# Kernel tuning notes

Hardware: AMD Instinct MI355X
Metric: run time of the kernel (lower is better)

Reference implementation:

```python
import jax, jax.numpy as jnp
import numpy as np

N_EMBD = 2048
D_FF = 4 * N_EMBD
BATCH, SEQ = 4, 2048
EPS = 1e-5


def rmsnorm(x):
    # RMSNorm without learned scale (BitNet reference BitLinear pre-norm)
    return x * jax.lax.rsqrt(jnp.mean(x * x, axis=-1, keepdims=True) + 1e-6)


def activation_quant(x):
    # per-token absmax 8-bit quantization
    scale = 127.0 / jnp.clip(jnp.max(jnp.abs(x), axis=-1, keepdims=True), EPS, None)
    return jnp.clip(jnp.round(x * scale), -128, 127) / scale


def weight_quant(w):
    # per-tensor absmean ternary quantization
    scale = 1.0 / jnp.clip(jnp.mean(jnp.abs(w)), EPS, None)
    return jnp.clip(jnp.round(w * scale), -1, 1) / scale


def bitlinear(x, w):
    # w: [out, in]; straight-through estimators for both quantizers
    xn = rmsnorm(x)
    xq = xn + jax.lax.stop_gradient(activation_quant(xn) - xn)
    wq = w + jax.lax.stop_gradient(weight_quant(w) - w)
    return jnp.einsum('bsi,oi->bso', xq, wq)


def setup_inputs() -> dict:
    key = jax.random.key(0)
    k0, k1, k2, k3 = jax.random.split(key, 4)
    x = jax.random.normal(k0, (BATCH, SEQ, N_EMBD), dtype=jnp.float32)
    s_in = 1.0 / np.sqrt(N_EMBD)
    s_ff = 1.0 / np.sqrt(D_FF)
    w1 = jax.random.normal(k1, (D_FF, N_EMBD), dtype=jnp.float32) * s_in
    w2 = jax.random.normal(k2, (D_FF, N_EMBD), dtype=jnp.float32) * s_in
    w3 = jax.random.normal(k3, (N_EMBD, D_FF), dtype=jnp.float32) * s_ff
    return {"x": x, "w1": w1, "w2": w2, "w3": w3}


def reference(x, w1, w2, w3):
    h = jax.nn.silu(bitlinear(x, w1)) * bitlinear(x, w2)  # [B,S,4E]
    return bitlinear(h, w3)  # [B,S,E]
```

## Files before the change

kernel.cpp:

```cpp
#include <hip/hip_runtime.h>
#include <cstdint>
#include <cstddef>

#define DEV __device__ __forceinline__

static constexpr float QEPS = 1e-5f;
static constexpr int   MTOK = 8192;
static constexpr int   EMB  = 2048;
static constexpr int   DFF  = 8192;
static constexpr int   MCH  = 2048;

typedef __attribute__((ext_vector_type(4))) int   i32x4;

DEV void async_cp16(const void* g, void* l) {
  __builtin_amdgcn_global_load_lds(
      (const __attribute__((address_space(1))) void*)g,
      (__attribute__((address_space(3))) void*)l, 16, 0, 0);
}

DEV void hard_barrier() {
  __builtin_amdgcn_sched_barrier(0);
  asm volatile("" ::: "memory");
  __builtin_amdgcn_s_barrier();
  asm volatile("" ::: "memory");
  __builtin_amdgcn_sched_barrier(0);
}

#define WAIT_VMCNT(N) do {                                   \
  __builtin_amdgcn_sched_barrier(0);                         \
  asm volatile("s_waitcnt vmcnt(" #N ")" ::: "memory");      \
  __builtin_amdgcn_sched_barrier(0);                         \
} while (0)

template<int PASSES>
DEV void stage128(const signed char* __restrict__ g, size_t ldb,
                  signed char* lds, int tid) {
  const int w  = tid >> 6, l = tid & 63;
  const int r8 = l >> 3;
  const int p  = l & 7;
  const int q  = p ^ r8;
#pragma unroll
  for (int it = 0; it < PASSES; ++it) {
    const int row = it * 64 + w * 8 + r8;
    async_cp16(g + (size_t)row * ldb + q * 16, lds + row * 128 + p * 16);
  }
}

DEV i32x4 lds_frag(const signed char* lds, int row, int s, int fq) {
  const int ch = ((s * 4 + fq) ^ (row & 7)) * 16;
  return *(const i32x4*)&lds[row * 128 + ch];
}

DEV float block_sum(float v) {
#pragma unroll
  for (int off = 32; off > 0; off >>= 1) v += __shfl_down(v, off);
  __shared__ float b[4];
  if ((threadIdx.x & 63) == 0) b[threadIdx.x >> 6] = v;
  __syncthreads();
  return (b[0] + b[1]) + (b[2] + b[3]);
}

DEV float block_max(float v) {
#pragma unroll
  for (int off = 32; off > 0; off >>= 1) v = fmaxf(v, __shfl_down(v, off));
  __shared__ float b[4];
  if ((threadIdx.x & 63) == 0) b[threadIdx.x >> 6] = v;
  __syncthreads();
  return fmaxf(fmaxf(b[0], b[1]), fmaxf(b[2], b[3]));
}

__global__ __launch_bounds__(256) void np_absmean_stage1(
    const float* __restrict__ w, float* __restrict__ partials) {
  const int t = threadIdx.x;
  const size_t leaf = (size_t)blockIdx.x * 256 + t;
  const float4* a4 = (const float4*)(w + leaf * 128);
  float L[16];
#pragma unroll
  for (int q = 0; q < 4; ++q) {
    float4 v0 = a4[q +  0];
    float4 v1 = a4[q +  4];
    float4 v2 = a4[q +  8];
    float4 v3 = a4[q + 12];
    float4 v4 = a4[q + 16];
    float4 v5 = a4[q + 20];
    float4 v6 = a4[q + 24];
    float4 v7 = a4[q + 28];
    L[4*q+0] = ((fabsf(v0.x)+fabsf(v1.x)) + (fabsf(v2.x)+fabsf(v3.x)))
             + ((fabsf(v4.x)+fabsf(v5.x)) + (fabsf(v6.x)+fabsf(v7.x)));
    L[4*q+1] = ((fabsf(v0.y)+fabsf(v1.y)) + (fabsf(v2.y)+fabsf(v3.y)))
             + ((fabsf(v4.y)+fabsf(v5.y)) + (fabsf(v6.y)+fabsf(v7.y)));
    L[4*q+2] = ((fabsf(v0.z)+fabsf(v1.z)) + (fabsf(v2.z)+fabsf(v3.z)))
             + ((fabsf(v4.z)+fabsf(v5.z)) + (fabsf(v6.z)+fabsf(v7.z)));
    L[4*q+3] = ((fabsf(v0.w)+fabsf(v1.w)) + (fabsf(v2.w)+fabsf(v3.w)))
             + ((fabsf(v4.w)+fabsf(v5.w)) + (fabsf(v6.w)+fabsf(v7.w)));
  }
#pragma unroll
  for (int l = 0; l < 8; ++l) L[l] += L[l + 8];
#pragma unroll
  for (int l = 0; l < 4; ++l) L[l] += L[l + 4];
  L[0] += L[2]; L[1] += L[3];
  const float res = L[0] + L[1];

  __shared__ float s[256];
  s[t] = res;
  __syncthreads();
  for (int width = 256; width > 1; width >>= 1) {
    const int half = width >> 1;
    float v = 0.f;
    if (t < half) v = s[2 * t] + s[2 * t + 1];
    __syncthreads();
    if (t < half) s[t] = v;
    __syncthreads();
  }
  if (t == 0) partials[blockIdx.x] = s[0];
}

__global__ __launch_bounds__(256) void np_absmean_stage2(
    const float* __restrict__ partials, float* __restrict__ out) {
  const int t = threadIdx.x;
  __shared__ float s[512];
  s[t] = partials[t];
  s[t + 256] = partials[t + 256];
  __syncthreads();
  for (int width = 512; width > 1; width >>= 1) {
    const int half = width >> 1;
    float v = 0.f;
    if (t < half) v = s[2 * t] + s[2 * t + 1];
    __syncthreads();
    if (t < half) s[t] = v;
    __syncthreads();
  }
  if (t == 0) out[0] = s[0];
}

__global__ __launch_bounds__(256) void quant_w_kernel(
    const float* __restrict__ w, signed char* __restrict__ wq,
    const float* __restrict__ sumf, size_t n4) {
  const double mean = (double)(*sumf) * (1.0 / 16777216.0);
  const double sc   = 1.0 / fmax(mean, (double)QEPS);
  const float4* w4 = (const float4*)w;
  int* o4 = (int*)wq;
  const size_t stride = (size_t)gridDim.x * blockDim.x;
  for (size_t i = (size_t)blockIdx.x * blockDim.x + threadIdx.x; i < n4; i += stride) {
    float4 v = w4[i];
    union { int i4; signed char c[4]; } p;
#pragma unroll
    for (int j = 0; j < 4; ++j) {
      const double pd = (double)(&v.x)[j] * sc;
      double r = fmin(fmax(rint(pd), -1.0), 1.0);
      if (fabs(fabs(pd) - 0.5) < 2e-7) r = (pd > 0.0) ? 0.5 : -0.5;
      p.c[j] = (signed char)(int)(2.0 * r);
    }
    o4[i] = p.i4;
  }
}

__global__ __launch_bounds__(256) void rms_quant_x_kernel(
    const float* __restrict__ x, signed char* __restrict__ xq,
    float* __restrict__ s_out) {
  const size_t row = blockIdx.x;
  const float* xr = x + row * EMB;
  const int t = threadIdx.x;
  float4 v0 = ((const float4*)xr)[t];
  float4 v1 = ((const float4*)xr)[t + 256];
  float vals[8] = {v0.x, v0.y, v0.z, v0.w, v1.x, v1.y, v1.z, v1.w};
  float ss = 0.f;
#pragma unroll
  for (int i = 0; i < 8; ++i) ss += vals[i] * vals[i];
  ss = block_sum(ss);
  const float r = 1.0f / sqrtf(ss * (1.0f / (float)EMB) + 1e-6f);
  float xn[8], am = 0.f;
#pragma unroll
  for (int i = 0; i < 8; ++i) { xn[i] = vals[i] * r; am = fmaxf(am, fabsf(xn[i])); }
  am = block_max(am);
  const float s = 127.0f / fmaxf(am, QEPS);
  union { int i; signed char c[4]; } p0, p1;
#pragma unroll
  for (int i = 0; i < 4; ++i) {
    p0.c[i] = (signed char)(int)fminf(fmaxf(rintf(xn[i]     * s), -128.f), 127.f);
    p1.c[i] = (signed char)(int)fminf(fmaxf(rintf(xn[4 + i] * s), -128.f), 127.f);
  }
  int* qr = (int*)(xq + row * EMB);
  qr[t]       = p0.i;
  qr[t + 256] = p1.i;
  if (t == 0) s_out[row] = s;
}

__global__ __launch_bounds__(256) void rms_quant_h_kernel(
    const float* __restrict__ H, signed char* __restrict__ hq,
    float* __restrict__ s_out) {
  const size_t row = blockIdx.x;
  const float* hr = H + row * (size_t)DFF;
  const int t = threadIdx.x;
  float vals[32];
#pragma unroll
  for (int k = 0; k < 8; ++k) {
    float4 v = ((const float4*)hr)[t + k * 256];
    vals[k * 4 + 0] = v.x; vals[k * 4 + 1] = v.y;
    vals[k * 4 + 2] = v.z; vals[k * 4 + 3] = v.w;
  }
  float ss = 0.f;
#pragma unroll
  for (int i = 0; i < 32; ++i) ss += vals[i] * vals[i];
  ss = block_sum(ss);
  const float r = 1.0f / sqrtf(ss * (1.0f / (float)DFF) + 1e-6f);
  float am = 0.f;
#pragma unroll
  for (int i = 0; i < 32; ++i) { vals[i] *= r; am = fmaxf(am, fabsf(vals[i])); }
  am = block_max(am);
  const float s = 127.0f / fmaxf(am, QEPS);
  int* qrow = (int*)(hq + row * (size_t)DFF);
#pragma unroll
  for (int k = 0; k < 8; ++k) {
    union { int i; signed char c[4]; } p;
#pragma unroll
    for (int j = 0; j < 4; ++j) {
      float q = fminf(fmaxf(rintf(vals[k * 4 + j] * s), -128.f), 127.f);
      p.c[j] = (signed char)(int)q;
    }
    qrow[t + k * 256] = p.i;
  }
  if (t == 0) s_out[row] = s;
}

__global__ __launch_bounds__(512, 1) void dual_gemm_silu_kernel(
    const signed char* __restrict__ Xq, const signed char* __restrict__ W1,
    const signed char* __restrict__ W2, float* __restrict__ H,
    const float* __restrict__ s_x, const float* __restrict__ wsum) {
  __shared__ alignas(16) signed char sA [2][256 * 128];
  __shared__ alignas(16) signed char sB1[2][128 * 128];
  __shared__ alignas(16) signed char sB2[2][128 * 128];
  const int tid = threadIdx.x;
  const int lane = tid & 63, wv = tid >> 6;
  const int wm = (wv >> 1) * 64, wn = (wv & 1) * 64;
  const int gx = gridDim.x;
  int lid = blockIdx.y * gx + blockIdx.x;
  const int cpx = (gx * gridDim.y) >> 3;
  lid = (lid & 7) * cpx + (lid >> 3);
  const int bm = (lid / gx) * 256, bn = (lid % gx) * 128;
  const int fr = lane & 15, fq = lane >> 4;

  i32x4 acc1[4][4] = {}, acc2[4][4] = {};

  stage128<4>(Xq + (size_t)bm * EMB, EMB, sA[0],  tid);
  stage128<2>(W1 + (size_t)bn * EMB, EMB, sB1[0], tid);
  stage128<2>(W2 + (size_t)bn * EMB, EMB, sB2[0], tid);

  constexpr int NKT = EMB / 128;
  int c = 0;
  for (int kt = 0; kt < NKT; ++kt) {
    if (kt + 1 < NKT) {
      const int ko = (kt + 1) * 128;
      stage128<4>(Xq + (size_t)bm * EMB + ko, EMB, sA[c ^ 1],  tid);
      stage128<2>(W1 + (size_t)bn * EMB + ko, EMB, sB1[c ^ 1], tid);
      stage128<2>(W2 + (size_t)bn * EMB + ko, EMB, sB2[c ^ 1], tid);
      WAIT_VMCNT(8);
    } else {
      WAIT_VMCNT(0);
    }
    hard_barrier();
    const signed char* a  = sA[c];
    const signed char* b1 = sB1[c];
    const signed char* b2 = sB2[c];
#pragma unroll
    for (int s = 0; s < 2; ++s) {
      i32x4 af[4], f1[4], f2[4];
#pragma unroll
      for (int i = 0; i < 4; ++i) af[i] = lds_frag(a,  wm + i * 16 + fr, s, fq);
#pragma unroll
      for (int j = 0; j < 4; ++j) {
        f1[j] = lds_frag(b1, wn + j * 16 + fr, s, fq);
        f2[j] = lds_frag(b2, wn + j * 16 + fr, s, fq);
      }
      __builtin_amdgcn_s_setprio(1);
#pragma unroll
      for (int i = 0; i < 4; ++i)
#pragma unroll
        for (int j = 0; j < 4; ++j) {
          acc1[i][j] = __builtin_amdgcn_mfma_i32_16x16x64_i8(af[i], f1[j], acc1[i][j], 0, 0, 0);
          acc2[i][j] = __builtin_amdgcn_mfma_i32_16x16x64_i8(af[i], f2[j], acc2[i][j], 0, 0, 0);
        }
      __builtin_amdgcn_s_setprio(0);
    }
    hard_barrier();
    c ^= 1;
  }

  const float sw1 = 1.0f / fmaxf(wsum[0] * (1.0f / 16777216.0f), QEPS);
  const float sw2 = 1.0f / fmaxf(wsum[1] * (1.0f / 16777216.0f), QEPS);
#pragma unroll
  for (int i = 0; i < 4; ++i) {
#pragma unroll
    for (int r = 0; r < 4; ++r) {
      const int m = bm + wm + i * 16 + fq * 4 + r;
      const float d1 = s_x[m] * sw1;
      const float d2 = s_x[m] * sw2;
#pragma unroll
      for (int j = 0; j < 4; ++j) {
        const float t1 = ((float)acc1[i][j][r] * 0.5f) / d1;
        const float t2 = ((float)acc2[i][j][r] * 0.5f) / d2;
        const float hv = (t1 / (1.0f + expf(-t1))) * t2;
        H[(size_t)m * DFF + (bn + wn + j * 16 + fr)] = hv;
      }
    }
  }
}

__global__ __launch_bounds__(512, 1) void gemm_out_kernel(
    const signed char* __restrict__ Aq, const signed char* __restrict__ B,
    float* __restrict__ C, const float* __restrict__ s_a,
    const float* __restrict__ wsum2) {
  __shared__ alignas(16) signed char sA[2][256 * 128];
  __shared__ alignas(16) signed char sB[2][256 * 128];
  const int tid = threadIdx.x;
  const int lane = tid & 63, wv = tid >> 6;
  const int wm = (wv >> 2) * 128, wn = (wv & 3) * 64;
  const int gx = gridDim.x;
  int lid = blockIdx.y * gx + blockIdx.x;
  const int cpx = (gx * gridDim.y) >> 3;
  lid = (lid & 7) * cpx + (lid >> 3);
  const int bm = (lid / gx) * 256, bn = (lid % gx) * 256;
  const int fr = lane & 15, fq = lane >> 4;

  i32x4 acc[8][4] = {};

  stage128<4>(Aq + (size_t)bm * DFF, DFF, sA[0], tid);
  stage128<4>(B  + (size_t)bn * DFF, DFF, sB[0], tid);

  constexpr int NKT = DFF / 128;
  int c = 0;
  for (int kt = 0; kt < NKT; ++kt) {
    if (kt + 1 < NKT) {
      const int ko = (kt + 1) * 128;
      stage128<4>(Aq + (size_t)bm * DFF + ko, DFF, sA[c ^ 1], tid);
      stage128<4>(B  + (size_t)bn * DFF + ko, DFF, sB[c ^ 1], tid);
      WAIT_VMCNT(8);
    } else {
      WAIT_VMCNT(0);
    }
    hard_barrier();
    const signed char* a = sA[c];
    const signed char* b = sB[c];
#pragma unroll
    for (int s = 0; s < 2; ++s) {
      i32x4 af[8], bf[4];
#pragma unroll
      for (int i = 0; i < 8; ++i) af[i] = lds_frag(a, wm + i * 16 + fr, s, fq);
#pragma unroll
      for (int j = 0; j < 4; ++j) bf[j] = lds_frag(b, wn + j * 16 + fr, s, fq);
      __builtin_amdgcn_s_setprio(1);
#pragma unroll
      for (int i = 0; i < 8; ++i)
#pragma unroll
        for (int j = 0; j < 4; ++j)
          acc[i][j] = __builtin_amdgcn_mfma_i32_16x16x64_i8(af[i], bf[j], acc[i][j], 0, 0, 0);
      __builtin_amdgcn_s_setprio(0);
    }
    hard_barrier();
    c ^= 1;
  }

  const float sw = 1.0f / fmaxf(wsum2[0] * (1.0f / 16777216.0f), QEPS);
#pragma unroll
  for (int i = 0; i < 8; ++i) {
#pragma unroll
    for (int r = 0; r < 4; ++r) {
      const int m = bm + wm + i * 16 + fq * 4 + r;
      const float d = s_a[m] * sw;
#pragma unroll
      for (int j = 0; j < 4; ++j)
        C[(size_t)m * EMB + (bn + wn + j * 16 + fr)] = ((float)acc[i][j][r] * 0.5f) / d;
    }
  }
}

extern "C" void kernel_launch(void* const* d_in, const int* in_sizes, int n_in,
                              void* d_out, int out_size, void* d_ws, size_t ws_size,
                              hipStream_t stream) {
  const float* x  = (const float*)d_in[0];
  const float* w1 = (const float*)d_in[1];
  const float* w2 = (const float*)d_in[2];
  const float* w3 = (const float*)d_in[3];
  float* out = (float*)d_out;

  const size_t NW = (size_t)DFF * EMB;
  const size_t MB = 1ull << 20;

  char* ws = (char*)d_ws;
  float* wsum = (float*)ws;
  float* s_x  = (float*)(ws + 4096);
  float* s_h  = (float*)(ws + 4096 + 32768);
  float* parts = (float*)(ws + 128 * 1024);
  signed char* xq  = (signed char*)(ws + MB);
  signed char* wq1 = (signed char*)(ws + 33 * MB);
  signed char* wq3 = wq1;
  signed char* wq2 = (signed char*)(ws + 65 * MB);
  signed char* hq  = (signed char*)(ws + 97 * MB);
  float* H = (float*)d_out;

  np_absmean_stage1<<<512, 256, 0, stream>>>(w1, parts);
  np_absmean_stage2<<<1, 256, 0, stream>>>(parts, wsum + 0);
  np_absmean_stage1<<<512, 256, 0, stream>>>(w2, parts + 512);
  np_absmean_stage2<<<1, 256, 0, stream>>>(parts + 512, wsum + 1);
  np_absmean_stage1<<<512, 256, 0, stream>>>(w3, parts + 1024);
  np_absmean_stage2<<<1, 256, 0, stream>>>(parts + 1024, wsum + 2);
  quant_w_kernel<<<1024, 256, 0, stream>>>(w1, wq1, wsum + 0, NW / 4);
  quant_w_kernel<<<1024, 256, 0, stream>>>(w2, wq2, wsum + 1, NW / 4);
  rms_quant_x_kernel<<<MTOK, 256, 0, stream>>>(x, xq, s_x);

  for (int c = 0; c < MTOK / MCH; ++c) {
    dual_gemm_silu_kernel<<<dim3(DFF / 128, MCH / 256), 512, 0, stream>>>(
        xq + (size_t)c * MCH * EMB, wq1, wq2, H, s_x + c * MCH, wsum);
    rms_quant_h_kernel<<<MCH, 256, 0, stream>>>(
        H, hq + (size_t)c * MCH * DFF, s_h + c * MCH);
  }

  quant_w_kernel<<<1024, 256, 0, stream>>>(w3, wq3, wsum + 2, NW / 4);
  gemm_out_kernel<<<dim3(EMB / 256, MTOK / 256), 512, 0, stream>>>(
      hq, wq3, out, s_h, wsum + 2);
}
```

Baseline: 883.9 us.

## Shrink GEMM blocks to 256 threads with K=64 stages for two blocks per CU

```diff
diff --git a/kernel.cpp b/kernel.cpp
--- a/kernel.cpp
+++ b/kernel.cpp
@@ -33,22 +33,22 @@
 } while (0)
 
 template<int PASSES>
-DEV void stage128(const signed char* __restrict__ g, size_t ldb,
-                  signed char* lds, int tid) {
+DEV void stage64(const signed char* __restrict__ g, size_t ldb,
+                 signed char* lds, int tid) {
   const int w  = tid >> 6, l = tid & 63;
-  const int r8 = l >> 3;
-  const int p  = l & 7;
-  const int q  = p ^ r8;
+  const int rr = w * 16 + (l >> 2);
+  const int p  = l & 3;
+  const int q  = p ^ ((l >> 3) & 3);
 #pragma unroll
   for (int it = 0; it < PASSES; ++it) {
-    const int row = it * 64 + w * 8 + r8;
-    async_cp16(g + (size_t)row * ldb + q * 16, lds + row * 128 + p * 16);
-  }
-}
-
-DEV i32x4 lds_frag(const signed char* lds, int row, int s, int fq) {
-  const int ch = ((s * 4 + fq) ^ (row & 7)) * 16;
-  return *(const i32x4*)&lds[row * 128 + ch];
+    const int row = it * 64 + rr;
+    async_cp16(g + (size_t)row * ldb + q * 16, lds + row * 64 + p * 16);
+  }
+}
+
+DEV i32x4 frag64(const signed char* lds, int row, int fq) {
+  const int ch = (fq ^ ((row >> 1) & 3)) << 4;
+  return *(const i32x4*)&lds[row * 64 + ch];
 }
 
 DEV float block_sum(float v) {
@@ -223,13 +223,13 @@
   if (t == 0) s_out[row] = s;
 }
 
-__global__ __launch_bounds__(512, 1) void dual_gemm_silu_kernel(
+__global__ __launch_bounds__(256, 2) void dual_gemm_silu_kernel(
     const signed char* __restrict__ Xq, const signed char* __restrict__ W1,
     const signed char* __restrict__ W2, float* __restrict__ H,
     const float* __restrict__ s_x, const float* __restrict__ wsum) {
-  __shared__ alignas(16) signed char sA [2][256 * 128];
-  __shared__ alignas(16) signed char sB1[2][128 * 128];
-  __shared__ alignas(16) signed char sB2[2][128 * 128];
+  __shared__ alignas(16) signed char sA [2][128 * 64];
+  __shared__ alignas(16) signed char sB1[2][128 * 64];
+  __shared__ alignas(16) signed char sB2[2][128 * 64];
   const int tid = threadIdx.x;
   const int lane = tid & 63, wv = tid >> 6;
   const int wm = (wv >> 1) * 64, wn = (wv & 1) * 64;
@@ -237,24 +237,24 @@
   int lid = blockIdx.y * gx + blockIdx.x;
   const int cpx = (gx * gridDim.y) >> 3;
   lid = (lid & 7) * cpx + (lid >> 3);
-  const int bm = (lid / gx) * 256, bn = (lid % gx) * 128;
+  const int bm = (lid / gx) * 128, bn = (lid % gx) * 128;
   const int fr = lane & 15, fq = lane >> 4;
 
   i32x4 acc1[4][4] = {}, acc2[4][4] = {};
 
-  stage128<4>(Xq + (size_t)bm * EMB, EMB, sA[0],  tid);
-  stage128<2>(W1 + (size_t)bn * EMB, EMB, sB1[0], tid);
-  stage128<2>(W2 + (size_t)bn * EMB, EMB, sB2[0], tid);
-
-  constexpr int NKT = EMB / 128;
+  stage64<2>(Xq + (size_t)bm * EMB, EMB, sA[0],  tid);
+  stage64<2>(W1 + (size_t)bn * EMB, EMB, sB1[0], tid);
+  stage64<2>(W2 + (size_t)bn * EMB, EMB, sB2[0], tid);
+
+  constexpr int NKT = EMB / 64;
   int c = 0;
   for (int kt = 0; kt < NKT; ++kt) {
     if (kt + 1 < NKT) {
-      const int ko = (kt + 1) * 128;
-      stage128<4>(Xq + (size_t)bm * EMB + ko, EMB, sA[c ^ 1],  tid);
-      stage128<2>(W1 + (size_t)bn * EMB + ko, EMB, sB1[c ^ 1], tid);
-      stage128<2>(W2 + (size_t)bn * EMB + ko, EMB, sB2[c ^ 1], tid);
-      WAIT_VMCNT(8);
+      const int ko = (kt + 1) * 64;
+      stage64<2>(Xq + (size_t)bm * EMB + ko, EMB, sA[c ^ 1],  tid);
+      stage64<2>(W1 + (size_t)bn * EMB + ko, EMB, sB1[c ^ 1], tid);
+      stage64<2>(W2 + (size_t)bn * EMB + ko, EMB, sB2[c ^ 1], tid);
+      WAIT_VMCNT(6);
     } else {
       WAIT_VMCNT(0);
     }
@@ -262,26 +262,23 @@
     const signed char* a  = sA[c];
     const signed char* b1 = sB1[c];
     const signed char* b2 = sB2[c];
-#pragma unroll
-    for (int s = 0; s < 2; ++s) {
-      i32x4 af[4], f1[4], f2[4];
-#pragma unroll
-      for (int i = 0; i < 4; ++i) af[i] = lds_frag(a,  wm + i * 16 + fr, s, fq);
+    i32x4 af[4], f1[4], f2[4];
+#pragma unroll
+    for (int i = 0; i < 4; ++i) af[i] = frag64(a,  wm + i * 16 + fr, fq);
+#pragma unroll
+    for (int j = 0; j < 4; ++j) {
+      f1[j] = frag64(b1, wn + j * 16 + fr, fq);
+      f2[j] = frag64(b2, wn + j * 16 + fr, fq);
+    }
+    __builtin_amdgcn_s_setprio(1);
+#pragma unroll
+    for (int i = 0; i < 4; ++i)
 #pragma unroll
       for (int j = 0; j < 4; ++j) {
-        f1[j] = lds_frag(b1, wn + j * 16 + fr, s, fq);
-        f2[j] = lds_frag(b2, wn + j * 16 + fr, s, fq);
+        acc1[i][j] = __builtin_amdgcn_mfma_i32_16x16x64_i8(af[i], f1[j], acc1[i][j], 0, 0, 0);
+        acc2[i][j] = __builtin_amdgcn_mfma_i32_16x16x64_i8(af[i], f2[j], acc2[i][j], 0, 0, 0);
       }
-      __builtin_amdgcn_s_setprio(1);
-#pragma unroll
-      for (int i = 0; i < 4; ++i)
-#pragma unroll
-        for (int j = 0; j < 4; ++j) {
-          acc1[i][j] = __builtin_amdgcn_mfma_i32_16x16x64_i8(af[i], f1[j], acc1[i][j], 0, 0, 0);
-          acc2[i][j] = __builtin_amdgcn_mfma_i32_16x16x64_i8(af[i], f2[j], acc2[i][j], 0, 0, 0);
-        }
-      __builtin_amdgcn_s_setprio(0);
-    }
+    __builtin_amdgcn_s_setprio(0);
     hard_barrier();
     c ^= 1;
   }
@@ -306,56 +303,53 @@
   }
 }
 
-__global__ __launch_bounds__(512, 1) void gemm_out_kernel(
+__global__ __launch_bounds__(256, 2) void gemm_out_kernel(
     const signed char* __restrict__ Aq, const signed char* __restrict__ B,
     float* __restrict__ C, const float* __restrict__ s_a,
     const float* __restrict__ wsum2) {
-  __shared__ alignas(16) signed char sA[2][256 * 128];
-  __shared__ alignas(16) signed char sB[2][256 * 128];
+  __shared__ alignas(16) signed char sA[2][256 * 64];
+  __shared__ alignas(16) signed char sB[2][128 * 64];
   const int tid = threadIdx.x;
   const int lane = tid & 63, wv = tid >> 6;
-  const int wm = (wv >> 2) * 128, wn = (wv & 3) * 64;
+  const int wm = (wv >> 1) * 128, wn = (wv & 1) * 64;
   const int gx = gridDim.x;
   int lid = blockIdx.y * gx + blockIdx.x;
   const int cpx = (gx * gridDim.y) >> 3;
   lid = (lid & 7) * cpx + (lid >> 3);
-  const int bm = (lid / gx) * 256, bn = (lid % gx) * 256;
+  const int bm = (lid / gx) * 256, bn = (lid % gx) * 128;
   const int fr = lane & 15, fq = lane >> 4;
 
   i32x4 acc[8][4] = {};
 
-  stage128<4>(Aq + (size_t)bm * DFF, DFF, sA[0], tid);
-  stage128<4>(B  + (size_t)bn * DFF, DFF, sB[0], tid);
-
-  constexpr int NKT = DFF / 128;
+  stage64<4>(Aq + (size_t)bm * DFF, DFF, sA[0], tid);
+  stage64<2>(B  + (size_t)bn * DFF, DFF, sB[0], tid);
+
+  constexpr int NKT = DFF / 64;
   int c = 0;
   for (int kt = 0; kt < NKT; ++kt) {
     if (kt + 1 < NKT) {
-      const int ko = (kt + 1) * 128;
-      stage128<4>(Aq + (size_t)bm * DFF + ko, DFF, sA[c ^ 1], tid);
-      stage128<4>(B  + (size_t)bn * DFF + ko, DFF, sB[c ^ 1], tid);
-      WAIT_VMCNT(8);
+      const int ko = (kt + 1) * 64;
+      stage64<4>(Aq + (size_t)bm * DFF + ko, DFF, sA[c ^ 1], tid);
+      stage64<2>(B  + (size_t)bn * DFF + ko, DFF, sB[c ^ 1], tid);
+      WAIT_VMCNT(6);
     } else {
       WAIT_VMCNT(0);
     }
     hard_barrier();
     const signed char* a = sA[c];
     const signed char* b = sB[c];
-#pragma unroll
-    for (int s = 0; s < 2; ++s) {
-      i32x4 af[8], bf[4];
-#pragma unroll
-      for (int i = 0; i < 8; ++i) af[i] = lds_frag(a, wm + i * 16 + fr, s, fq);
-#pragma unroll
-      for (int j = 0; j < 4; ++j) bf[j] = lds_frag(b, wn + j * 16 + fr, s, fq);
-      __builtin_amdgcn_s_setprio(1);
-#pragma unroll
-      for (int i = 0; i < 8; ++i)
-#pragma unroll
-        for (int j = 0; j < 4; ++j)
-          acc[i][j] = __builtin_amdgcn_mfma_i32_16x16x64_i8(af[i], bf[j], acc[i][j], 0, 0, 0);
-      __builtin_amdgcn_s_setprio(0);
-    }
+    i32x4 af[8], bf[4];
+#pragma unroll
+    for (int i = 0; i < 8; ++i) af[i] = frag64(a, wm + i * 16 + fr, fq);
+#pragma unroll
+    for (int j = 0; j < 4; ++j) bf[j] = frag64(b, wn + j * 16 + fr, fq);
+    __builtin_amdgcn_s_setprio(1);
+#pragma unroll
+    for (int i = 0; i < 8; ++i)
+#pragma unroll
+      for (int j = 0; j < 4; ++j)
+        acc[i][j] = __builtin_amdgcn_mfma_i32_16x16x64_i8(af[i], bf[j], acc[i][j], 0, 0, 0);
+    __builtin_amdgcn_s_setprio(0);
     hard_barrier();
     c ^= 1;
   }
@@ -409,13 +403,13 @@
   rms_quant_x_kernel<<<MTOK, 256, 0, stream>>>(x, xq, s_x);
 
   for (int c = 0; c < MTOK / MCH; ++c) {
-    dual_gemm_silu_kernel<<<dim3(DFF / 128, MCH / 256), 512, 0, stream>>>(
+    dual_gemm_silu_kernel<<<dim3(DFF / 128, MCH / 128), 256, 0, stream>>>(
         xq + (size_t)c * MCH * EMB, wq1, wq2, H, s_x + c * MCH, wsum);
     rms_quant_h_kernel<<<MCH, 256, 0, stream>>>(
         H, hq + (size_t)c * MCH * DFF, s_h + c * MCH);
   }
 
   quant_w_kernel<<<1024, 256, 0, stream>>>(w3, wq3, wsum + 2, NW / 4);
-  gemm_out_kernel<<<dim3(EMB / 256, MTOK / 256), 512, 0, stream>>>(
+  gemm_out_kernel<<<dim3(EMB / 128, MTOK / 256), 256, 0, stream>>>(
       hq, wq3, out, s_h, wsum + 2);
 }
```

New measurement: 923.3 us. 4.5% more time.

## Shrink dual-GEMM tile to 128x128, single-buffer K=64, two blocks per CU

Applied to the files above, without the earlier changes.

```diff
diff --git a/kernel.cpp b/kernel.cpp
--- a/kernel.cpp
+++ b/kernel.cpp
@@ -31,6 +31,19 @@
   asm volatile("s_waitcnt vmcnt(" #N ")" ::: "memory");      \
   __builtin_amdgcn_sched_barrier(0);                         \
 } while (0)
+
+DEV void stage_tile64(const signed char* __restrict__ g, size_t ldb,
+                      signed char* lds, int tid) {
+  const int w  = tid >> 6, l = tid & 63;
+  const int rr = w * 16 + (l >> 2);
+  const int p  = l & 3;
+  const int q  = p ^ ((l >> 3) & 3);
+#pragma unroll
+  for (int it = 0; it < 2; ++it) {
+    const int r = it * 64 + rr;
+    async_cp16(g + (size_t)r * ldb + q * 16, lds + r * 64 + p * 16);
+  }
+}
 
 template<int PASSES>
 DEV void stage128(const signed char* __restrict__ g, size_t ldb,
@@ -223,67 +236,44 @@
   if (t == 0) s_out[row] = s;
 }
 
-__global__ __launch_bounds__(512, 1) void dual_gemm_silu_kernel(
+__global__ __launch_bounds__(256, 2) void dual_gemm_silu_kernel(
     const signed char* __restrict__ Xq, const signed char* __restrict__ W1,
     const signed char* __restrict__ W2, float* __restrict__ H,
     const float* __restrict__ s_x, const float* __restrict__ wsum) {
-  __shared__ alignas(16) signed char sA [2][256 * 128];
-  __shared__ alignas(16) signed char sB1[2][128 * 128];
-  __shared__ alignas(16) signed char sB2[2][128 * 128];
+  __shared__ alignas(16) signed char sA [128 * 64];
+  __shared__ alignas(16) signed char sB1[128 * 64];
+  __shared__ alignas(16) signed char sB2[128 * 64];
   const int tid = threadIdx.x;
   const int lane = tid & 63, wv = tid >> 6;
   const int wm = (wv >> 1) * 64, wn = (wv & 1) * 64;
-  const int gx = gridDim.x;
-  int lid = blockIdx.y * gx + blockIdx.x;
-  const int cpx = (gx * gridDim.y) >> 3;
-  lid = (lid & 7) * cpx + (lid >> 3);
-  const int bm = (lid / gx) * 256, bn = (lid % gx) * 128;
+  const int bm = blockIdx.y * 128, bn = blockIdx.x * 128;
   const int fr = lane & 15, fq = lane >> 4;
+  const int ch = (fq ^ ((fr >> 1) & 3)) * 16;
 
   i32x4 acc1[4][4] = {}, acc2[4][4] = {};
 
-  stage128<4>(Xq + (size_t)bm * EMB, EMB, sA[0],  tid);
-  stage128<2>(W1 + (size_t)bn * EMB, EMB, sB1[0], tid);
-  stage128<2>(W2 + (size_t)bn * EMB, EMB, sB2[0], tid);
-
-  constexpr int NKT = EMB / 128;
-  int c = 0;
-  for (int kt = 0; kt < NKT; ++kt) {
-    if (kt + 1 < NKT) {
-      const int ko = (kt + 1) * 128;
-      stage128<4>(Xq + (size_t)bm * EMB + ko, EMB, sA[c ^ 1],  tid);
-      stage128<2>(W1 + (size_t)bn * EMB + ko, EMB, sB1[c ^ 1], tid);
-      stage128<2>(W2 + (size_t)bn * EMB + ko, EMB, sB2[c ^ 1], tid);
-      WAIT_VMCNT(8);
-    } else {
-      WAIT_VMCNT(0);
-    }
-    hard_barrier();
-    const signed char* a  = sA[c];
-    const signed char* b1 = sB1[c];
-    const signed char* b2 = sB2[c];
-#pragma unroll
-    for (int s = 0; s < 2; ++s) {
-      i32x4 af[4], f1[4], f2[4];
-#pragma unroll
-      for (int i = 0; i < 4; ++i) af[i] = lds_frag(a,  wm + i * 16 + fr, s, fq);
+  for (int k0 = 0; k0 < EMB; k0 += 64) {
+    stage_tile64(Xq + (size_t)bm * EMB + k0, EMB, sA,  tid);
+    stage_tile64(W1 + (size_t)bn * EMB + k0, EMB, sB1, tid);
+    stage_tile64(W2 + (size_t)bn * EMB + k0, EMB, sB2, tid);
+    __syncthreads();
+    i32x4 af[4], f1[4], f2[4];
+#pragma unroll
+    for (int i = 0; i < 4; ++i)
+      af[i] = *(const i32x4*)&sA[(wm + i * 16 + fr) * 64 + ch];
+#pragma unroll
+    for (int j = 0; j < 4; ++j) {
+      f1[j] = *(const i32x4*)&sB1[(wn + j * 16 + fr) * 64 + ch];
+      f2[j] = *(const i32x4*)&sB2[(wn + j * 16 + fr) * 64 + ch];
+    }
+#pragma unroll
+    for (int i = 0; i < 4; ++i)
 #pragma unroll
       for (int j = 0; j < 4; ++j) {
-        f1[j] = lds_frag(b1, wn + j * 16 + fr, s, fq);
-        f2[j] = lds_frag(b2, wn + j * 16 + fr, s, fq);
+        acc1[i][j] = __builtin_amdgcn_mfma_i32_16x16x64_i8(af[i], f1[j], acc1[i][j], 0, 0, 0);
+        acc2[i][j] = __builtin_amdgcn_mfma_i32_16x16x64_i8(af[i], f2[j], acc2[i][j], 0, 0, 0);
       }
-      __builtin_amdgcn_s_setprio(1);
-#pragma unroll
-      for (int i = 0; i < 4; ++i)
-#pragma unroll
-        for (int j = 0; j < 4; ++j) {
-          acc1[i][j] = __builtin_amdgcn_mfma_i32_16x16x64_i8(af[i], f1[j], acc1[i][j], 0, 0, 0);
-          acc2[i][j] = __builtin_amdgcn_mfma_i32_16x16x64_i8(af[i], f2[j], acc2[i][j], 0, 0, 0);
-        }
-      __builtin_amdgcn_s_setprio(0);
-    }
-    hard_barrier();
-    c ^= 1;
+    __syncthreads();
   }
 
   const float sw1 = 1.0f / fmaxf(wsum[0] * (1.0f / 16777216.0f), QEPS);
@@ -293,14 +283,14 @@
 #pragma unroll
     for (int r = 0; r < 4; ++r) {
       const int m = bm + wm + i * 16 + fq * 4 + r;
-      const float d1 = s_x[m] * sw1;
-      const float d2 = s_x[m] * sw2;
+      const float id1 = 0.5f / (s_x[m] * sw1);
+      const float id2 = 0.5f / (s_x[m] * sw2);
 #pragma unroll
       for (int j = 0; j < 4; ++j) {
-        const float t1 = ((float)acc1[i][j][r] * 0.5f) / d1;
-        const float t2 = ((float)acc2[i][j][r] * 0.5f) / d2;
-        const float hv = (t1 / (1.0f + expf(-t1))) * t2;
-        H[(size_t)m * DFF + (bn + wn + j * 16 + fr)] = hv;
+        const float t1 = (float)acc1[i][j][r] * id1;
+        const float t2 = (float)acc2[i][j][r] * id2;
+        const float sig = __builtin_amdgcn_rcpf(1.0f + __expf(-t1));
+        H[(size_t)m * DFF + (bn + wn + j * 16 + fr)] = t1 * sig * t2;
       }
     }
   }
@@ -366,10 +356,10 @@
 #pragma unroll
     for (int r = 0; r < 4; ++r) {
       const int m = bm + wm + i * 16 + fq * 4 + r;
-      const float d = s_a[m] * sw;
+      const float id = 0.5f / (s_a[m] * sw);
 #pragma unroll
       for (int j = 0; j < 4; ++j)
-        C[(size_t)m * EMB + (bn + wn + j * 16 + fr)] = ((float)acc[i][j][r] * 0.5f) / d;
+        C[(size_t)m * EMB + (bn + wn + j * 16 + fr)] = (float)acc[i][j][r] * id;
     }
   }
 }
@@ -409,7 +399,7 @@
   rms_quant_x_kernel<<<MTOK, 256, 0, stream>>>(x, xq, s_x);
 
   for (int c = 0; c < MTOK / MCH; ++c) {
-    dual_gemm_silu_kernel<<<dim3(DFF / 128, MCH / 256), 512, 0, stream>>>(
+    dual_gemm_silu_kernel<<<dim3(DFF / 128, MCH / 128), 256, 0, stream>>>(
         xq + (size_t)c * MCH * EMB, wq1, wq2, H, s_x + c * MCH, wsum);
     rms_quant_h_kernel<<<MCH, 256, 0, stream>>>(
         H, hq + (size_t)c * MCH * DFF, s_h + c * MCH);
```

Measured after the change: 804.2 us. 9.0% less time.
